# Performance work log

Measured on AMD Instinct MI355X. Metric: run time of the kernel, lower is better.

Reference implementation:

```python
import jax, jax.numpy as jnp
import numpy as np

N = 100000   # num_nodes
E = 1000000  # num_edges
H = 64       # h_dim
OUT = 16     # out_dim (num classes)
R = 90       # num_rels
B = 8        # num_bases


def setup_inputs() -> dict:
    key = jax.random.key(0)
    ks = jax.random.split(key, 16)
    feats = jax.random.normal(ks[0], (N, H), dtype=jnp.float32)
    src = jax.random.randint(ks[1], (E,), 0, N)
    dst = jax.random.randint(ks[2], (E,), 0, N)
    etype = jax.random.randint(ks[3], (E,), 0, R)
    norm = jax.random.uniform(ks[4], (E, 1), dtype=jnp.float32)
    s_in = 1.0 / np.sqrt(H)
    s_b = 1.0 / np.sqrt(B)
    # layer 0: H->H, layer 1 (hidden): H->H, layer 2: H->OUT
    coeff0 = jax.random.normal(ks[5], (R, B), dtype=jnp.float32) * s_b
    bases0 = jax.random.normal(ks[6], (B, H, H), dtype=jnp.float32) * s_in
    bias0 = jnp.zeros((H,), dtype=jnp.float32)
    coeff1 = jax.random.normal(ks[7], (R, B), dtype=jnp.float32) * s_b
    bases1 = jax.random.normal(ks[8], (B, H, H), dtype=jnp.float32) * s_in
    bias1 = jnp.zeros((H,), dtype=jnp.float32)
    coeff2 = jax.random.normal(ks[9], (R, B), dtype=jnp.float32) * s_b
    bases2 = jax.random.normal(ks[10], (B, H, OUT), dtype=jnp.float32) * s_in
    bias2 = jnp.zeros((OUT,), dtype=jnp.float32)
    return {
        "feats": feats,
        "coeff0": coeff0, "bases0": bases0, "bias0": bias0,
        "coeff1": coeff1, "bases1": bases1, "bias1": bias1,
        "coeff2": coeff2, "bases2": bases2, "bias2": bias2,
        "src": src, "dst": dst, "etype": etype, "norm": norm,
    }


def _rgcn_layer(x, coeff, bases, bias, src, dst, etype, norm, relu):
    # Basis decomposition: W_r = sum_b coeff[r,b] * bases[b]
    # Project all nodes through every basis once: [N, B, out]
    Hn = jnp.einsum('ni,bio->nbo', x, bases)
    c = coeff[etype]  # [E, B] per-edge basis coefficients
    # Per-edge message m_e = (sum_b c_eb * Hn[src_e, b]) * norm_e,
    # accumulated over the (small, fixed) basis dim to avoid an [E,B,out] buffer.
    m = c[:, 0:1] * Hn[src, 0]
    for b in range(1, bases.shape[0]):
        m = m + c[:, b:b + 1] * Hn[src, b]
    m = m * norm
    h = jax.ops.segment_sum(m, dst, num_segments=x.shape[0]) + bias
    return jax.nn.relu(h) if relu else h


def reference(feats, coeff0, bases0, bias0, coeff1, bases1, bias1,
              coeff2, bases2, bias2, src, dst, etype, norm):
    h = _rgcn_layer(feats, coeff0, bases0, bias0, src, dst, etype, norm, relu=True)
    h = _rgcn_layer(h, coeff1, bases1, bias1, src, dst, etype, norm, relu=True)
    h = _rgcn_layer(h, coeff2, bases2, bias2, src, dst, etype, norm, relu=False)
    return h
```

## Files before the change

kernel.cpp:

```cpp
#include <hip/hip_runtime.h>
#include <hip/hip_bf16.h>
#include <cstdint>

#define NNODES 100000
#define NEDGES 1000000
#define HDIM 64
#define ODIM 16
#define NB 8
#define KDIM (HDIM * NB)

typedef short short8 __attribute__((ext_vector_type(8)));
typedef float f32x4  __attribute__((ext_vector_type(4)));
union FragU { uint4 u; short8 s; };

__device__ __forceinline__ float asf(uint32_t u) { float f; __builtin_memcpy(&f, &u, 4); return f; }
__device__ __forceinline__ uint32_t asu(float f) { uint32_t u; __builtin_memcpy(&u, &f, 4); return u; }
__device__ __forceinline__ uint16_t f2bf(float f) {
    uint32_t x = asu(f);
    return (uint16_t)((x + 0x7FFFu + ((x >> 16) & 1u)) >> 16);
}
__device__ __forceinline__ uint32_t pack2(float lo, float hi) {
    return (uint32_t)f2bf(lo) | ((uint32_t)f2bf(hi) << 16);
}
__device__ __forceinline__ void fmaC(const float4& cA, const float4& cB, float xs,
                                     float* __restrict__ acc) {
    acc[0] = fmaf(cA.x, xs, acc[0]); acc[1] = fmaf(cA.y, xs, acc[1]);
    acc[2] = fmaf(cA.z, xs, acc[2]); acc[3] = fmaf(cA.w, xs, acc[3]);
    acc[4] = fmaf(cB.x, xs, acc[4]); acc[5] = fmaf(cB.y, xs, acc[5]);
    acc[6] = fmaf(cB.z, xs, acc[6]); acc[7] = fmaf(cB.w, xs, acc[7]);
}

__global__ void cast_kernel(const float* __restrict__ in, uint16_t* __restrict__ out, int n4) {
    const int stride = (int)(gridDim.x * blockDim.x);
    for (int idx = (int)(blockIdx.x * blockDim.x + threadIdx.x); idx < n4; idx += stride) {
        float4 v = reinterpret_cast<const float4*>(in)[idx];
        uint2 p;
        p.x = pack2(v.x, v.y);
        p.y = pack2(v.z, v.w);
        reinterpret_cast<uint2*>(out)[idx] = p;
    }
}

__global__ void zero_kernel(int* __restrict__ p, int n) {
    for (int i = (int)(blockIdx.x * blockDim.x + threadIdx.x); i < n;
         i += (int)(gridDim.x * blockDim.x)) p[i] = 0;
}

__global__ void hist_kernel(const int* __restrict__ dst, int* __restrict__ cnt, int nE) {
    for (int e = (int)(blockIdx.x * blockDim.x + threadIdx.x); e < nE;
         e += (int)(gridDim.x * blockDim.x)) atomicAdd(&cnt[dst[e]], 1);
}

#define SCAN_B 512
__launch_bounds__(SCAN_B)
__global__ void scan_partial_kernel(const int* __restrict__ cnt, int* __restrict__ bsum, int n) {
    __shared__ int sh[SCAN_B];
    int id = (int)(blockIdx.x * SCAN_B + threadIdx.x);
    sh[threadIdx.x] = (id < n) ? cnt[id] : 0;
    __syncthreads();
    for (int off = SCAN_B / 2; off > 0; off >>= 1) {
        if ((int)threadIdx.x < off) sh[threadIdx.x] += sh[threadIdx.x + off];
        __syncthreads();
    }
    if (threadIdx.x == 0) bsum[blockIdx.x] = sh[0];
}

__launch_bounds__(256)
__global__ void scan_base_kernel(const int* __restrict__ bsum, int* __restrict__ bbase,
                                 int* __restrict__ offs, int nblk, int nNodes) {
    __shared__ int sh[256];
    const int t = (int)threadIdx.x;
    int v = (t < nblk) ? bsum[t] : 0;
    sh[t] = v;
    __syncthreads();
    for (int off = 1; off < 256; off <<= 1) {
        int tmp = (t >= off) ? sh[t - off] : 0;
        __syncthreads();
        sh[t] += tmp;
        __syncthreads();
    }
    if (t < nblk) bbase[t] = sh[t] - v;
    if (t == 255) offs[nNodes] = sh[255];
}

__launch_bounds__(SCAN_B)
__global__ void scan_final_kernel(int* __restrict__ cnt, const int* __restrict__ bbase,
                                  int* __restrict__ offs, int n) {
    __shared__ int sh[SCAN_B];
    int id = (int)(blockIdx.x * SCAN_B + threadIdx.x);
    int v = (id < n) ? cnt[id] : 0;
    sh[threadIdx.x] = v;
    __syncthreads();
    for (int off = 1; off < SCAN_B; off <<= 1) {
        int tmp = ((int)threadIdx.x >= off) ? sh[threadIdx.x - off] : 0;
        __syncthreads();
        sh[threadIdx.x] += tmp;
        __syncthreads();
    }
    if (id < n) {
        int excl = sh[threadIdx.x] - v + bbase[blockIdx.x];
        offs[id] = excl;
        cnt[id]  = excl;
    }
}

__global__ void scatter_kernel(const int* __restrict__ src, const int* __restrict__ dst,
                               const int* __restrict__ et, const float* __restrict__ norm,
                               int* __restrict__ cursor, uint2* __restrict__ rec, int nE) {
    for (int e = (int)(blockIdx.x * blockDim.x + threadIdx.x); e < nE;
         e += (int)(gridDim.x * blockDim.x)) {
        int p = atomicAdd(&cursor[dst[e]], 1);
        rec[p] = make_uint2((uint32_t)src[e] | ((uint32_t)et[e] << 20), asu(norm[e]));
    }
}

__launch_bounds__(256)
__global__ void csr_agg_kernel(const uint16_t* __restrict__ x,
                               const float* __restrict__ coeff,
                               const int* __restrict__ offs,
                               const uint2* __restrict__ rec,
                               uint16_t* __restrict__ G, int nNodes) {
    const int hl   = (int)threadIdx.x & 31;
    const int hwid = (int)((blockIdx.x * blockDim.x + threadIdx.x) >> 5);
    const int nhw  = (int)((gridDim.x * blockDim.x) >> 5);
    for (int d = hwid; d < nNodes; d += nhw) {
        const int j0 = offs[d], j1 = offs[d + 1];
        float accL[NB] = {0.f, 0.f, 0.f, 0.f, 0.f, 0.f, 0.f, 0.f};
        float accH[NB] = {0.f, 0.f, 0.f, 0.f, 0.f, 0.f, 0.f, 0.f};
        int j = j0;
        for (; j + 4 <= j1; j += 4) {
            const uint2 r0 = rec[j];
            const uint2 r1 = rec[j + 1];
            const uint2 r2 = rec[j + 2];
            const uint2 r3 = rec[j + 3];
            const uint32_t w0 = *reinterpret_cast<const uint32_t*>(
                x + (size_t)(r0.x & 0xFFFFFu) * HDIM + 2 * hl);
            const uint32_t w1 = *reinterpret_cast<const uint32_t*>(
                x + (size_t)(r1.x & 0xFFFFFu) * HDIM + 2 * hl);
            const uint32_t w2 = *reinterpret_cast<const uint32_t*>(
                x + (size_t)(r2.x & 0xFFFFFu) * HDIM + 2 * hl);
            const uint32_t w3 = *reinterpret_cast<const uint32_t*>(
                x + (size_t)(r3.x & 0xFFFFFu) * HDIM + 2 * hl);

            {
                const float4 cA = *reinterpret_cast<const float4*>(coeff + (r0.x >> 20) * NB);
                const float4 cB = *reinterpret_cast<const float4*>(coeff + (r0.x >> 20) * NB + 4);
                const float nm = asf(r0.y);
                fmaC(cA, cB, asf(w0 << 16) * nm, accL);
                fmaC(cA, cB, asf(w0 & 0xFFFF0000u) * nm, accH);
            }
            {
                const float4 cA = *reinterpret_cast<const float4*>(coeff + (r1.x >> 20) * NB);
                const float4 cB = *reinterpret_cast<const float4*>(coeff + (r1.x >> 20) * NB + 4);
                const float nm = asf(r1.y);
                fmaC(cA, cB, asf(w1 << 16) * nm, accL);
                fmaC(cA, cB, asf(w1 & 0xFFFF0000u) * nm, accH);
            }
            {
                const float4 cA = *reinterpret_cast<const float4*>(coeff + (r2.x >> 20) * NB);
                const float4 cB = *reinterpret_cast<const float4*>(coeff + (r2.x >> 20) * NB + 4);
                const float nm = asf(r2.y);
                fmaC(cA, cB, asf(w2 << 16) * nm, accL);
                fmaC(cA, cB, asf(w2 & 0xFFFF0000u) * nm, accH);
            }
            {
                const float4 cA = *reinterpret_cast<const float4*>(coeff + (r3.x >> 20) * NB);
                const float4 cB = *reinterpret_cast<const float4*>(coeff + (r3.x >> 20) * NB + 4);
                const float nm = asf(r3.y);
                fmaC(cA, cB, asf(w3 << 16) * nm, accL);
                fmaC(cA, cB, asf(w3 & 0xFFFF0000u) * nm, accH);
            }
        }
        for (; j < j1; j++) {
            const uint2 r0 = rec[j];
            const uint32_t w0 = *reinterpret_cast<const uint32_t*>(
                x + (size_t)(r0.x & 0xFFFFFu) * HDIM + 2 * hl);
            const float4 cA = *reinterpret_cast<const float4*>(coeff + (r0.x >> 20) * NB);
            const float4 cB = *reinterpret_cast<const float4*>(coeff + (r0.x >> 20) * NB + 4);
            const float nm = asf(r0.y);
            fmaC(cA, cB, asf(w0 << 16) * nm, accL);
            fmaC(cA, cB, asf(w0 & 0xFFFF0000u) * nm, accH);
        }
        uint4 lo, hi;
        lo.x = pack2(accL[0], accL[1]); lo.y = pack2(accL[2], accL[3]);
        lo.z = pack2(accL[4], accL[5]); lo.w = pack2(accL[6], accL[7]);
        hi.x = pack2(accH[0], accH[1]); hi.y = pack2(accH[2], accH[3]);
        hi.z = pack2(accH[4], accH[5]); hi.w = pack2(accH[6], accH[7]);
        uint16_t* gp = G + (size_t)d * KDIM + hl * 16;
        *reinterpret_cast<uint4*>(gp)     = lo;
        *reinterpret_cast<uint4*>(gp + 8) = hi;
    }
}

__launch_bounds__(256)
__global__ void proj_hidden_kernel(const uint16_t* __restrict__ G,
                                   const float* __restrict__ bases,
                                   const float* __restrict__ bias,
                                   uint16_t* __restrict__ xout, int nNodes) {
    constexpr int OT = HDIM / 16;
    __shared__ __align__(16) uint16_t Wf[16 * OT * 64 * 8];

    const int t    = (int)threadIdx.x;
    const int lane = t & 63;
    const int w    = t >> 6;
    const int q    = lane >> 4;
    const int c    = lane & 15;

    for (int idx = t; idx < 16 * OT * 64 * 8; idx += 256) {
        int j    = idx & 7;
        int ln   = (idx >> 3) & 63;
        int rest = idx >> 9;
        int ot   = rest & (OT - 1);
        int kb   = rest >> 2;
        int k    = kb * 32 + (ln >> 4) * 8 + j;
        int o    = ot * 16 + (ln & 15);
        int i    = k >> 3, b = k & 7;
        Wf[idx] = f2bf(bases[(size_t)(b * HDIM + i) * HDIM + o]);
    }
    __syncthreads();

    float bv[OT];
#pragma unroll
    for (int ot = 0; ot < OT; ot++) bv[ot] = bias[ot * 16 + c];

    const int nTiles = (nNodes + 63) / 64;
    for (int tile = blockIdx.x; tile < nTiles; tile += gridDim.x) {
        const int n0w = tile * 64 + w * 16;
        int arow = n0w + c;
        if (arow > nNodes - 1) arow = nNodes - 1;
        const uint16_t* gp = G + (size_t)arow * KDIM + q * 8;

        f32x4 acc[OT];
#pragma unroll
        for (int ot = 0; ot < OT; ot++) acc[ot] = {0.f, 0.f, 0.f, 0.f};

#pragma unroll
        for (int kb = 0; kb < 16; kb++) {
            FragU a;
            a.u = *reinterpret_cast<const uint4*>(gp + kb * 32);
#pragma unroll
            for (int ot = 0; ot < OT; ot++) {
                FragU b;
                b.u = *reinterpret_cast<const uint4*>(Wf + ((kb * OT + ot) * 64 + lane) * 8);
                acc[ot] = __builtin_amdgcn_mfma_f32_16x16x32_bf16(a.s, b.s, acc[ot], 0, 0, 0);
            }
        }

#pragma unroll
        for (int r = 0; r < 4; r++) {
            const int node = n0w + q * 4 + r;
            if (node < nNodes) {
#pragma unroll
                for (int ot = 0; ot < OT; ot++) {
                    float v = fmaxf(acc[ot][r] + bv[ot], 0.f);
                    xout[(size_t)node * HDIM + ot * 16 + c] = f2bf(v);
                }
            }
        }
    }
}

__launch_bounds__(256)
__global__ void proj_out_kernel(const uint16_t* __restrict__ G,
                                const float* __restrict__ bases,
                                const float* __restrict__ bias,
                                float* __restrict__ out, int nNodes) {
    __shared__ __align__(16) uint16_t Wf[16 * 64 * 8];

    const int t    = (int)threadIdx.x;
    const int lane = t & 63;
    const int w    = t >> 6;
    const int q    = lane >> 4;
    const int c    = lane & 15;

    for (int idx = t; idx < 16 * 64 * 8; idx += 256) {
        int j  = idx & 7;
        int ln = (idx >> 3) & 63;
        int kb = idx >> 9;
        int k  = kb * 32 + (ln >> 4) * 8 + j;
        int o  = ln & 15;
        int i  = k >> 3, b = k & 7;
        Wf[idx] = f2bf(bases[(size_t)(b * HDIM + i) * ODIM + o]);
    }
    __syncthreads();

    const float bv = bias[c];

    const int nTiles = (nNodes + 63) / 64;
    for (int tile = blockIdx.x; tile < nTiles; tile += gridDim.x) {
        const int n0w = tile * 64 + w * 16;
        int arow = n0w + c;
        if (arow > nNodes - 1) arow = nNodes - 1;
        const uint16_t* gp = G + (size_t)arow * KDIM + q * 8;

        f32x4 acc = {0.f, 0.f, 0.f, 0.f};
#pragma unroll
        for (int kb = 0; kb < 16; kb++) {
            FragU a, b;
            a.u = *reinterpret_cast<const uint4*>(gp + kb * 32);
            b.u = *reinterpret_cast<const uint4*>(Wf + (kb * 64 + lane) * 8);
            acc = __builtin_amdgcn_mfma_f32_16x16x32_bf16(a.s, b.s, acc, 0, 0, 0);
        }

#pragma unroll
        for (int r = 0; r < 4; r++) {
            const int node = n0w + q * 4 + r;
            if (node < nNodes) out[(size_t)node * ODIM + c] = acc[r] + bv;
        }
    }
}

extern "C" void kernel_launch(void* const* d_in, const int* in_sizes, int n_in,
                              void* d_out, int out_size, void* d_ws, size_t ws_size,
                              hipStream_t stream) {
    const float* feats  = (const float*)d_in[0];
    const float* coeff0 = (const float*)d_in[1];
    const float* bases0 = (const float*)d_in[2];
    const float* bias0  = (const float*)d_in[3];
    const float* coeff1 = (const float*)d_in[4];
    const float* bases1 = (const float*)d_in[5];
    const float* bias1  = (const float*)d_in[6];
    const float* coeff2 = (const float*)d_in[7];
    const float* bases2 = (const float*)d_in[8];
    const float* bias2  = (const float*)d_in[9];
    const int*   src    = (const int*)d_in[10];
    const int*   dst    = (const int*)d_in[11];
    const int*   etype  = (const int*)d_in[12];
    const float* norm   = (const float*)d_in[13];
    float* out = (float*)d_out;

    char* base = (char*)d_ws;
    uint16_t* G = (uint16_t*)base;
    uint16_t* x = (uint16_t*)(base + (size_t)NNODES * KDIM * 2);
    const size_t OFF_OFFS  = 115200000;
    const size_t OFF_CURS  = OFF_OFFS + 400016;
    const size_t OFF_BSUM  = OFF_CURS + 400016;
    const size_t OFF_BBASE = OFF_BSUM + 1024;
    const size_t OFF_REC   = OFF_BBASE + 1024;
    int*   offs  = (int*)(base + OFF_OFFS);
    int*   curs  = (int*)(base + OFF_CURS);
    int*   bsum  = (int*)(base + OFF_BSUM);
    int*   bbase = (int*)(base + OFF_BBASE);
    uint2* rec   = (uint2*)(base + OFF_REC);

    const int nblk = (NNODES + SCAN_B - 1) / SCAN_B;

    hipLaunchKernelGGL(zero_kernel, dim3(256), dim3(256), 0, stream, curs, NNODES);
    hipLaunchKernelGGL(hist_kernel, dim3(2048), dim3(256), 0, stream, dst, curs, NEDGES);
    hipLaunchKernelGGL(scan_partial_kernel, dim3(nblk), dim3(SCAN_B), 0, stream, curs, bsum, NNODES);
    hipLaunchKernelGGL(scan_base_kernel, dim3(1), dim3(256), 0, stream, bsum, bbase, offs, nblk, NNODES);
    hipLaunchKernelGGL(scan_final_kernel, dim3(nblk), dim3(SCAN_B), 0, stream, curs, bbase, offs, NNODES);
    hipLaunchKernelGGL(scatter_kernel, dim3(2048), dim3(256), 0, stream,
                       src, dst, etype, norm, curs, rec, NEDGES);

    hipLaunchKernelGGL(cast_kernel, dim3(2048), dim3(256), 0, stream,
                       feats, x, NNODES * HDIM / 4);

    hipLaunchKernelGGL(csr_agg_kernel, dim3(2048), dim3(256), 0, stream,
                       x, coeff0, offs, rec, G, NNODES);
    hipLaunchKernelGGL(proj_hidden_kernel, dim3(512), dim3(256), 0, stream,
                       G, bases0, bias0, x, NNODES);
    hipLaunchKernelGGL(csr_agg_kernel, dim3(2048), dim3(256), 0, stream,
                       x, coeff1, offs, rec, G, NNODES);
    hipLaunchKernelGGL(proj_hidden_kernel, dim3(512), dim3(256), 0, stream,
                       G, bases1, bias1, x, NNODES);
    hipLaunchKernelGGL(csr_agg_kernel, dim3(2048), dim3(256), 0, stream,
                       x, coeff2, offs, rec, G, NNODES);
    hipLaunchKernelGGL(proj_out_kernel, dim3(512), dim3(256), 0, stream,
                       G, bases2, bias2, out, NNODES);
}
```

Measured before the change: 534.2 us.

## Fuse CSR gather aggregation with MFMA basis projection via shared-memory tile

Merges the per-node gather/aggregate kernel and the basis projection GEMM into one kernel per layer. Each 1024-thread block aggregates 64 destination nodes into a swizzled LDS tile and then runs MFMA on it. This removes the write and reread of the large [N, 512] bf16 intermediate in global memory. It adds block-wide barriers and uses large blocks with about 80KB of LDS, which may limit occupancy and let slow nodes with many edges stall their whole block. Ping-pong buffers xA and xB replace the in-place x update.

```diff
diff --git a/kernel.cpp b/kernel.cpp
--- a/kernel.cpp
+++ b/kernel.cpp
@@ -8,6 +8,7 @@
 #define ODIM 16
 #define NB 8
 #define KDIM (HDIM * NB)
+#define TILE 64
 
 typedef short short8 __attribute__((ext_vector_type(8)));
 typedef float f32x4  __attribute__((ext_vector_type(4)));
@@ -114,166 +115,171 @@
     }
 }
 
-__launch_bounds__(256)
-__global__ void csr_agg_kernel(const uint16_t* __restrict__ x,
-                               const float* __restrict__ coeff,
-                               const int* __restrict__ offs,
-                               const uint2* __restrict__ rec,
-                               uint16_t* __restrict__ G, int nNodes) {
-    const int hl   = (int)threadIdx.x & 31;
-    const int hwid = (int)((blockIdx.x * blockDim.x + threadIdx.x) >> 5);
-    const int nhw  = (int)((gridDim.x * blockDim.x) >> 5);
-    for (int d = hwid; d < nNodes; d += nhw) {
-        const int j0 = offs[d], j1 = offs[d + 1];
-        float accL[NB] = {0.f, 0.f, 0.f, 0.f, 0.f, 0.f, 0.f, 0.f};
-        float accH[NB] = {0.f, 0.f, 0.f, 0.f, 0.f, 0.f, 0.f, 0.f};
-        int j = j0;
-        for (; j + 4 <= j1; j += 4) {
-            const uint2 r0 = rec[j];
-            const uint2 r1 = rec[j + 1];
-            const uint2 r2 = rec[j + 2];
-            const uint2 r3 = rec[j + 3];
-            const uint32_t w0 = *reinterpret_cast<const uint32_t*>(
-                x + (size_t)(r0.x & 0xFFFFFu) * HDIM + 2 * hl);
-            const uint32_t w1 = *reinterpret_cast<const uint32_t*>(
-                x + (size_t)(r1.x & 0xFFFFFu) * HDIM + 2 * hl);
-            const uint32_t w2 = *reinterpret_cast<const uint32_t*>(
-                x + (size_t)(r2.x & 0xFFFFFu) * HDIM + 2 * hl);
-            const uint32_t w3 = *reinterpret_cast<const uint32_t*>(
-                x + (size_t)(r3.x & 0xFFFFFu) * HDIM + 2 * hl);
-
-            {
-                const float4 cA = *reinterpret_cast<const float4*>(coeff + (r0.x >> 20) * NB);
-                const float4 cB = *reinterpret_cast<const float4*>(coeff + (r0.x >> 20) * NB + 4);
-                const float nm = asf(r0.y);
-                fmaC(cA, cB, asf(w0 << 16) * nm, accL);
-                fmaC(cA, cB, asf(w0 & 0xFFFF0000u) * nm, accH);
-            }
-            {
-                const float4 cA = *reinterpret_cast<const float4*>(coeff + (r1.x >> 20) * NB);
-                const float4 cB = *reinterpret_cast<const float4*>(coeff + (r1.x >> 20) * NB + 4);
-                const float nm = asf(r1.y);
-                fmaC(cA, cB, asf(w1 << 16) * nm, accL);
-                fmaC(cA, cB, asf(w1 & 0xFFFF0000u) * nm, accH);
-            }
-            {
-                const float4 cA = *reinterpret_cast<const float4*>(coeff + (r2.x >> 20) * NB);
-                const float4 cB = *reinterpret_cast<const float4*>(coeff + (r2.x >> 20) * NB + 4);
-                const float nm = asf(r2.y);
-                fmaC(cA, cB, asf(w2 << 16) * nm, accL);
-                fmaC(cA, cB, asf(w2 & 0xFFFF0000u) * nm, accH);
-            }
-            {
-                const float4 cA = *reinterpret_cast<const float4*>(coeff + (r3.x >> 20) * NB);
-                const float4 cB = *reinterpret_cast<const float4*>(coeff + (r3.x >> 20) * NB + 4);
-                const float nm = asf(r3.y);
-                fmaC(cA, cB, asf(w3 << 16) * nm, accL);
-                fmaC(cA, cB, asf(w3 & 0xFFFF0000u) * nm, accH);
-            }
-        }
-        for (; j < j1; j++) {
-            const uint2 r0 = rec[j];
-            const uint32_t w0 = *reinterpret_cast<const uint32_t*>(
-                x + (size_t)(r0.x & 0xFFFFFu) * HDIM + 2 * hl);
+__device__ __forceinline__ void gather_node(const uint16_t* __restrict__ x,
+                                            const float* __restrict__ coeff,
+                                            const uint2* __restrict__ rec,
+                                            int j0, int j1, int hl,
+                                            float* __restrict__ accL,
+                                            float* __restrict__ accH) {
+    int j = j0;
+    for (; j + 4 <= j1; j += 4) {
+        const uint2 r0 = rec[j];
+        const uint2 r1 = rec[j + 1];
+        const uint2 r2 = rec[j + 2];
+        const uint2 r3 = rec[j + 3];
+        const uint32_t w0 = *reinterpret_cast<const uint32_t*>(
+            x + (size_t)(r0.x & 0xFFFFFu) * HDIM + 2 * hl);
+        const uint32_t w1 = *reinterpret_cast<const uint32_t*>(
+            x + (size_t)(r1.x & 0xFFFFFu) * HDIM + 2 * hl);
+        const uint32_t w2 = *reinterpret_cast<const uint32_t*>(
+            x + (size_t)(r2.x & 0xFFFFFu) * HDIM + 2 * hl);
+        const uint32_t w3 = *reinterpret_cast<const uint32_t*>(
+            x + (size_t)(r3.x & 0xFFFFFu) * HDIM + 2 * hl);
+        {
             const float4 cA = *reinterpret_cast<const float4*>(coeff + (r0.x >> 20) * NB);
             const float4 cB = *reinterpret_cast<const float4*>(coeff + (r0.x >> 20) * NB + 4);
             const float nm = asf(r0.y);
             fmaC(cA, cB, asf(w0 << 16) * nm, accL);
             fmaC(cA, cB, asf(w0 & 0xFFFF0000u) * nm, accH);
         }
-        uint4 lo, hi;
-        lo.x = pack2(accL[0], accL[1]); lo.y = pack2(accL[2], accL[3]);
-        lo.z = pack2(accL[4], accL[5]); lo.w = pack2(accL[6], accL[7]);
-        hi.x = pack2(accH[0], accH[1]); hi.y = pack2(accH[2], accH[3]);
-        hi.z = pack2(accH[4], accH[5]); hi.w = pack2(accH[6], accH[7]);
-        uint16_t* gp = G + (size_t)d * KDIM + hl * 16;
-        *reinterpret_cast<uint4*>(gp)     = lo;
-        *reinterpret_cast<uint4*>(gp + 8) = hi;
-    }
-}
-
-__launch_bounds__(256)
-__global__ void proj_hidden_kernel(const uint16_t* __restrict__ G,
-                                   const float* __restrict__ bases,
-                                   const float* __restrict__ bias,
-                                   uint16_t* __restrict__ xout, int nNodes) {
+        {
+            const float4 cA = *reinterpret_cast<const float4*>(coeff + (r1.x >> 20) * NB);
+            const float4 cB = *reinterpret_cast<const float4*>(coeff + (r1.x >> 20) * NB + 4);
+            const float nm = asf(r1.y);
+            fmaC(cA, cB, asf(w1 << 16) * nm, accL);
+            fmaC(cA, cB, asf(w1 & 0xFFFF0000u) * nm, accH);
+        }
+        {
+            const float4 cA = *reinterpret_cast<const float4*>(coeff + (r2.x >> 20) * NB);
+            const float4 cB = *reinterpret_cast<const float4*>(coeff + (r2.x >> 20) * NB + 4);
+            const float nm = asf(r2.y);
+            fmaC(cA, cB, asf(w2 << 16) * nm, accL);
+            fmaC(cA, cB, asf(w2 & 0xFFFF0000u) * nm, accH);
+        }
+        {
+            const float4 cA = *reinterpret_cast<const float4*>(coeff + (r3.x >> 20) * NB);
+            const float4 cB = *reinterpret_cast<const float4*>(coeff + (r3.x >> 20) * NB + 4);
+            const float nm = asf(r3.y);
+            fmaC(cA, cB, asf(w3 << 16) * nm, accL);
+            fmaC(cA, cB, asf(w3 & 0xFFFF0000u) * nm, accH);
+        }
+    }
+    for (; j < j1; j++) {
+        const uint2 r0 = rec[j];
+        const uint32_t w0 = *reinterpret_cast<const uint32_t*>(
+            x + (size_t)(r0.x & 0xFFFFFu) * HDIM + 2 * hl);
+        const float4 cA = *reinterpret_cast<const float4*>(coeff + (r0.x >> 20) * NB);
+        const float4 cB = *reinterpret_cast<const float4*>(coeff + (r0.x >> 20) * NB + 4);
+        const float nm = asf(r0.y);
+        fmaC(cA, cB, asf(w0 << 16) * nm, accL);
+        fmaC(cA, cB, asf(w0 & 0xFFFF0000u) * nm, accH);
+    }
+}
+
+__launch_bounds__(1024)
+__global__ void fused_hidden_kernel(const uint16_t* __restrict__ x,
+                                    const float* __restrict__ coeff,
+                                    const float* __restrict__ bases,
+                                    const float* __restrict__ bias,
+                                    const int* __restrict__ offs,
+                                    const uint2* __restrict__ rec,
+                                    uint16_t* __restrict__ xout, int nNodes) {
     constexpr int OT = HDIM / 16;
     __shared__ __align__(16) uint16_t Wf[16 * OT * 64 * 8];
+    __shared__ __align__(16) uint16_t Gs[TILE * KDIM];
 
     const int t    = (int)threadIdx.x;
     const int lane = t & 63;
     const int w    = t >> 6;
+    const int hw   = t >> 5;
+    const int hl   = t & 31;
     const int q    = lane >> 4;
     const int c    = lane & 15;
-
-    for (int idx = t; idx < 16 * OT * 64 * 8; idx += 256) {
+    const int rt   = w & 3;
+    const int ot   = w >> 2;
+
+    for (int idx = t; idx < 16 * OT * 64 * 8; idx += 1024) {
         int j    = idx & 7;
         int ln   = (idx >> 3) & 63;
         int rest = idx >> 9;
-        int ot   = rest & (OT - 1);
+        int o_t  = rest & (OT - 1);
         int kb   = rest >> 2;
         int k    = kb * 32 + (ln >> 4) * 8 + j;
-        int o    = ot * 16 + (ln & 15);
+        int o    = o_t * 16 + (ln & 15);
         int i    = k >> 3, b = k & 7;
         Wf[idx] = f2bf(bases[(size_t)(b * HDIM + i) * HDIM + o]);
     }
-    __syncthreads();
-
-    float bv[OT];
-#pragma unroll
-    for (int ot = 0; ot < OT; ot++) bv[ot] = bias[ot * 16 + c];
-
-    const int nTiles = (nNodes + 63) / 64;
-    for (int tile = blockIdx.x; tile < nTiles; tile += gridDim.x) {
-        const int n0w = tile * 64 + w * 16;
-        int arow = n0w + c;
-        if (arow > nNodes - 1) arow = nNodes - 1;
-        const uint16_t* gp = G + (size_t)arow * KDIM + q * 8;
-
-        f32x4 acc[OT];
-#pragma unroll
-        for (int ot = 0; ot < OT; ot++) acc[ot] = {0.f, 0.f, 0.f, 0.f};
-
+
+    const float bv = bias[ot * 16 + c];
+    const int rsw  = rt * 16 + c;
+    const uint16_t* arow = Gs + rsw * KDIM;
+    const int sw   = rsw & 7;
+
+    const int nTiles = (nNodes + TILE - 1) / TILE;
+    for (int tile = (int)blockIdx.x; tile < nTiles; tile += (int)gridDim.x) {
+#pragma unroll
+        for (int s = 0; s < 2; s++) {
+            const int r = hw * 2 + s;
+            const int d = tile * TILE + r;
+            if (d < nNodes) {
+                float accL[NB] = {0.f, 0.f, 0.f, 0.f, 0.f, 0.f, 0.f, 0.f};
+                float accH[NB] = {0.f, 0.f, 0.f, 0.f, 0.f, 0.f, 0.f, 0.f};
+                gather_node(x, coeff, rec, offs[d], offs[d + 1], hl, accL, accH);
+                uint4 lo, hi;
+                lo.x = pack2(accL[0], accL[1]); lo.y = pack2(accL[2], accL[3]);
+                lo.z = pack2(accL[4], accL[5]); lo.w = pack2(accL[6], accL[7]);
+                hi.x = pack2(accH[0], accH[1]); hi.y = pack2(accH[2], accH[3]);
+                hi.z = pack2(accH[4], accH[5]); hi.w = pack2(accH[6], accH[7]);
+                uint16_t* gp = Gs + r * KDIM;
+                *reinterpret_cast<uint4*>(gp + ((hl ^ (r & 7)) * 8))        = lo;
+                *reinterpret_cast<uint4*>(gp + (((32 + hl) ^ (r & 7)) * 8)) = hi;
+            }
+        }
+        __syncthreads();
+
+        f32x4 acc = {0.f, 0.f, 0.f, 0.f};
 #pragma unroll
         for (int kb = 0; kb < 16; kb++) {
-            FragU a;
-            a.u = *reinterpret_cast<const uint4*>(gp + kb * 32);
-#pragma unroll
-            for (int ot = 0; ot < OT; ot++) {
-                FragU b;
-                b.u = *reinterpret_cast<const uint4*>(Wf + ((kb * OT + ot) * 64 + lane) * 8);
-                acc[ot] = __builtin_amdgcn_mfma_f32_16x16x32_bf16(a.s, b.s, acc[ot], 0, 0, 0);
-            }
-        }
-
-#pragma unroll
-        for (int r = 0; r < 4; r++) {
-            const int node = n0w + q * 4 + r;
+            const int g0 = (q & 1) * 32 + 2 * kb + (q >> 1);
+            FragU a, b;
+            a.u = *reinterpret_cast<const uint4*>(arow + ((g0 ^ sw) * 8));
+            b.u = *reinterpret_cast<const uint4*>(Wf + ((kb * OT + ot) * 64 + lane) * 8);
+            acc = __builtin_amdgcn_mfma_f32_16x16x32_bf16(a.s, b.s, acc, 0, 0, 0);
+        }
+
+        const int nbase = tile * TILE + rt * 16 + q * 4;
+#pragma unroll
+        for (int ri = 0; ri < 4; ri++) {
+            const int node = nbase + ri;
             if (node < nNodes) {
-#pragma unroll
-                for (int ot = 0; ot < OT; ot++) {
-                    float v = fmaxf(acc[ot][r] + bv[ot], 0.f);
-                    xout[(size_t)node * HDIM + ot * 16 + c] = f2bf(v);
-                }
-            }
-        }
-    }
-}
-
-__launch_bounds__(256)
-__global__ void proj_out_kernel(const uint16_t* __restrict__ G,
-                                const float* __restrict__ bases,
-                                const float* __restrict__ bias,
-                                float* __restrict__ out, int nNodes) {
+                float v = fmaxf(acc[ri] + bv, 0.f);
+                xout[(size_t)node * HDIM + ot * 16 + c] = f2bf(v);
+            }
+        }
+        __syncthreads();
+    }
+}
+
+__launch_bounds__(1024)
+__global__ void fused_out_kernel(const uint16_t* __restrict__ x,
+                                 const float* __restrict__ coeff,
+                                 const float* __restrict__ bases,
+                                 const float* __restrict__ bias,
+                                 const int* __restrict__ offs,
+                                 const uint2* __restrict__ rec,
+                                 float* __restrict__ out, int nNodes) {
     __shared__ __align__(16) uint16_t Wf[16 * 64 * 8];
+    __shared__ __align__(16) uint16_t Gs[TILE * KDIM];
 
     const int t    = (int)threadIdx.x;
     const int lane = t & 63;
     const int w    = t >> 6;
+    const int hw   = t >> 5;
+    const int hl   = t & 31;
     const int q    = lane >> 4;
     const int c    = lane & 15;
 
-    for (int idx = t; idx < 16 * 64 * 8; idx += 256) {
+    for (int idx = t; idx < 16 * 64 * 8; idx += 1024) {
         int j  = idx & 7;
         int ln = (idx >> 3) & 63;
         int kb = idx >> 9;
@@ -282,31 +288,53 @@
         int i  = k >> 3, b = k & 7;
         Wf[idx] = f2bf(bases[(size_t)(b * HDIM + i) * ODIM + o]);
     }
-    __syncthreads();
 
     const float bv = bias[c];
-
-    const int nTiles = (nNodes + 63) / 64;
-    for (int tile = blockIdx.x; tile < nTiles; tile += gridDim.x) {
-        const int n0w = tile * 64 + w * 16;
-        int arow = n0w + c;
-        if (arow > nNodes - 1) arow = nNodes - 1;
-        const uint16_t* gp = G + (size_t)arow * KDIM + q * 8;
-
-        f32x4 acc = {0.f, 0.f, 0.f, 0.f};
-#pragma unroll
-        for (int kb = 0; kb < 16; kb++) {
-            FragU a, b;
-            a.u = *reinterpret_cast<const uint4*>(gp + kb * 32);
-            b.u = *reinterpret_cast<const uint4*>(Wf + (kb * 64 + lane) * 8);
-            acc = __builtin_amdgcn_mfma_f32_16x16x32_bf16(a.s, b.s, acc, 0, 0, 0);
-        }
-
-#pragma unroll
-        for (int r = 0; r < 4; r++) {
-            const int node = n0w + q * 4 + r;
-            if (node < nNodes) out[(size_t)node * ODIM + c] = acc[r] + bv;
-        }
+    const int rt   = w & 3;
+    const int rsw  = rt * 16 + c;
+    const uint16_t* arow = Gs + rsw * KDIM;
+    const int sw   = rsw & 7;
+
+    const int nTiles = (nNodes + TILE - 1) / TILE;
+    for (int tile = (int)blockIdx.x; tile < nTiles; tile += (int)gridDim.x) {
+#pragma unroll
+        for (int s = 0; s < 2; s++) {
+            const int r = hw * 2 + s;
+            const int d = tile * TILE + r;
+            if (d < nNodes) {
+                float accL[NB] = {0.f, 0.f, 0.f, 0.f, 0.f, 0.f, 0.f, 0.f};
+                float accH[NB] = {0.f, 0.f, 0.f, 0.f, 0.f, 0.f, 0.f, 0.f};
+                gather_node(x, coeff, rec, offs[d], offs[d + 1], hl, accL, accH);
+                uint4 lo, hi;
+                lo.x = pack2(accL[0], accL[1]); lo.y = pack2(accL[2], accL[3]);
+                lo.z = pack2(accL[4], accL[5]); lo.w = pack2(accL[6], accL[7]);
+                hi.x = pack2(accH[0], accH[1]); hi.y = pack2(accH[2], accH[3]);
+                hi.z = pack2(accH[4], accH[5]); hi.w = pack2(accH[6], accH[7]);
+                uint16_t* gp = Gs + r * KDIM;
+                *reinterpret_cast<uint4*>(gp + ((hl ^ (r & 7)) * 8))        = lo;
+                *reinterpret_cast<uint4*>(gp + (((32 + hl) ^ (r & 7)) * 8)) = hi;
+            }
+        }
+        __syncthreads();
+
+        if (w < 4) {
+            f32x4 acc = {0.f, 0.f, 0.f, 0.f};
+#pragma unroll
+            for (int kb = 0; kb < 16; kb++) {
+                const int g0 = (q & 1) * 32 + 2 * kb + (q >> 1);
+                FragU a, b;
+                a.u = *reinterpret_cast<const uint4*>(arow + ((g0 ^ sw) * 8));
+                b.u = *reinterpret_cast<const uint4*>(Wf + ((kb * 64 + lane) * 8));
+                acc = __builtin_amdgcn_mfma_f32_16x16x32_bf16(a.s, b.s, acc, 0, 0, 0);
+            }
+            const int nbase = tile * TILE + rt * 16 + q * 4;
+#pragma unroll
+            for (int ri = 0; ri < 4; ri++) {
+                const int node = nbase + ri;
+                if (node < nNodes) out[(size_t)node * ODIM + c] = acc[ri] + bv;
+            }
+        }
+        __syncthreads();
     }
 }
 
@@ -330,8 +358,8 @@
     float* out = (float*)d_out;
 
     char* base = (char*)d_ws;
-    uint16_t* G = (uint16_t*)base;
-    uint16_t* x = (uint16_t*)(base + (size_t)NNODES * KDIM * 2);
+    uint16_t* xA = (uint16_t*)base;
+    uint16_t* xB = (uint16_t*)(base + (size_t)NNODES * HDIM * 2);
     const size_t OFF_OFFS  = 115200000;
     const size_t OFF_CURS  = OFF_OFFS + 400016;
     const size_t OFF_BSUM  = OFF_CURS + 400016;
@@ -354,18 +382,12 @@
                        src, dst, etype, norm, curs, rec, NEDGES);
 
     hipLaunchKernelGGL(cast_kernel, dim3(2048), dim3(256), 0, stream,
-                       feats, x, NNODES * HDIM / 4);
-
-    hipLaunchKernelGGL(csr_agg_kernel, dim3(2048), dim3(256), 0, stream,
-                       x, coeff0, offs, rec, G, NNODES);
-    hipLaunchKernelGGL(proj_hidden_kernel, dim3(512), dim3(256), 0, stream,
-                       G, bases0, bias0, x, NNODES);
-    hipLaunchKernelGGL(csr_agg_kernel, dim3(2048), dim3(256), 0, stream,
-                       x, coeff1, offs, rec, G, NNODES);
-    hipLaunchKernelGGL(proj_hidden_kernel, dim3(512), dim3(256), 0, stream,
-                       G, bases1, bias1, x, NNODES);
-    hipLaunchKernelGGL(csr_agg_kernel, dim3(2048), dim3(256), 0, stream,
-                       x, coeff2, offs, rec, G, NNODES);
-    hipLaunchKernelGGL(proj_out_kernel, dim3(512), dim3(256), 0, stream,
-                       G, bases2, bias2, out, NNODES);
-}
+                       feats, xA, NNODES * HDIM / 4);
+
+    hipLaunchKernelGGL(fused_hidden_kernel, dim3(512), dim3(1024), 0, stream,
+                       xA, coeff0, bases0, bias0, offs, rec, xB, NNODES);
+    hipLaunchKernelGGL(fused_hidden_kernel, dim3(512), dim3(1024), 0, stream,
+                       xB, coeff1, bases1, bias1, offs, rec, xA, NNODES);
+    hipLaunchKernelGGL(fused_out_kernel, dim3(512), dim3(1024), 0, stream,
+                       xA, coeff2, bases2, bias2, offs, rec, out, NNODES);
+}
```

New measurement: 537.0 us. No clear change (+0.5%).

## Hold projection weights in registers and split output tiles across waves

Applied to the files above, without the earlier changes.

The projection kernels stop staging bf16 basis weights in LDS and instead load each wave's B fragments straight into registers. In proj_hidden each wave now owns one 16-column output tile and loops over four 16-row node groups, rather than each wave computing all four output tiles for its own rows. Launch bounds gain a minimum-occupancy hint and the grids double to 1024 blocks. The goal is to drop LDS reads and the setup barrier, at the cost of higher register pressure and each wave reading the G rows four times (likely served by cache).

```diff
diff --git a/kernel.cpp b/kernel.cpp
--- a/kernel.cpp
+++ b/kernel.cpp
@@ -7,6 +7,7 @@
 #define HDIM 64
 #define ODIM 16
 #define NB 8
+#define NREL 90
 #define KDIM (HDIM * NB)
 
 typedef short short8 __attribute__((ext_vector_type(8)));
@@ -192,119 +193,99 @@
     }
 }
 
-__launch_bounds__(256)
+__launch_bounds__(256, 3)
 __global__ void proj_hidden_kernel(const uint16_t* __restrict__ G,
                                    const float* __restrict__ bases,
                                    const float* __restrict__ bias,
                                    uint16_t* __restrict__ xout, int nNodes) {
-    constexpr int OT = HDIM / 16;
-    __shared__ __align__(16) uint16_t Wf[16 * OT * 64 * 8];
-
+    const int t    = (int)threadIdx.x;
+    const int lane = t & 63;
+    const int ot   = t >> 6;
+    const int q    = lane >> 4;
+    const int c    = lane & 15;
+
+    FragU bf[16];
+#pragma unroll
+    for (int kb = 0; kb < 16; kb++) {
+#pragma unroll
+        for (int j = 0; j < 8; j++) {
+            const int k = kb * 32 + q * 8 + j;
+            const int i = k >> 3, b = k & 7;
+            bf[kb].s[j] = (short)f2bf(bases[(size_t)(b * HDIM + i) * HDIM + ot * 16 + c]);
+        }
+    }
+    const float bv = bias[ot * 16 + c];
+
+    const int nTiles = (nNodes + 63) / 64;
+    for (int tile = (int)blockIdx.x; tile < nTiles; tile += (int)gridDim.x) {
+#pragma unroll
+        for (int g = 0; g < 4; g++) {
+            int arow = tile * 64 + g * 16 + c;
+            if (arow > nNodes - 1) arow = nNodes - 1;
+            const uint16_t* gp = G + (size_t)arow * KDIM + q * 8;
+
+            f32x4 acc = {0.f, 0.f, 0.f, 0.f};
+#pragma unroll
+            for (int kb = 0; kb < 16; kb++) {
+                FragU a;
+                a.u = *reinterpret_cast<const uint4*>(gp + kb * 32);
+                acc = __builtin_amdgcn_mfma_f32_16x16x32_bf16(a.s, bf[kb].s, acc, 0, 0, 0);
+            }
+
+            const int nbase = tile * 64 + g * 16 + q * 4;
+#pragma unroll
+            for (int r = 0; r < 4; r++) {
+                const int node = nbase + r;
+                if (node < nNodes) {
+                    float v = fmaxf(acc[r] + bv, 0.f);
+                    xout[(size_t)node * HDIM + ot * 16 + c] = f2bf(v);
+                }
+            }
+        }
+    }
+}
+
+__launch_bounds__(256, 3)
+__global__ void proj_out_kernel(const uint16_t* __restrict__ G,
+                                const float* __restrict__ bases,
+                                const float* __restrict__ bias,
+                                float* __restrict__ out, int nNodes) {
     const int t    = (int)threadIdx.x;
     const int lane = t & 63;
     const int w    = t >> 6;
     const int q    = lane >> 4;
     const int c    = lane & 15;
 
-    for (int idx = t; idx < 16 * OT * 64 * 8; idx += 256) {
-        int j    = idx & 7;
-        int ln   = (idx >> 3) & 63;
-        int rest = idx >> 9;
-        int ot   = rest & (OT - 1);
-        int kb   = rest >> 2;
-        int k    = kb * 32 + (ln >> 4) * 8 + j;
-        int o    = ot * 16 + (ln & 15);
-        int i    = k >> 3, b = k & 7;
-        Wf[idx] = f2bf(bases[(size_t)(b * HDIM + i) * HDIM + o]);
-    }
-    __syncthreads();
-
-    float bv[OT];
-#pragma unroll
-    for (int ot = 0; ot < OT; ot++) bv[ot] = bias[ot * 16 + c];
+    FragU bf[16];
+#pragma unroll
+    for (int kb = 0; kb < 16; kb++) {
+#pragma unroll
+        for (int j = 0; j < 8; j++) {
+            const int k = kb * 32 + q * 8 + j;
+            const int i = k >> 3, b = k & 7;
+            bf[kb].s[j] = (short)f2bf(bases[(size_t)(b * HDIM + i) * ODIM + c]);
+        }
+    }
+    const float bv = bias[c];
 
     const int nTiles = (nNodes + 63) / 64;
-    for (int tile = blockIdx.x; tile < nTiles; tile += gridDim.x) {
-        const int n0w = tile * 64 + w * 16;
-        int arow = n0w + c;
+    for (int tile = (int)blockIdx.x; tile < nTiles; tile += (int)gridDim.x) {
+        int arow = tile * 64 + w * 16 + c;
         if (arow > nNodes - 1) arow = nNodes - 1;
         const uint16_t* gp = G + (size_t)arow * KDIM + q * 8;
 
-        f32x4 acc[OT];
-#pragma unroll
-        for (int ot = 0; ot < OT; ot++) acc[ot] = {0.f, 0.f, 0.f, 0.f};
-
+        f32x4 acc = {0.f, 0.f, 0.f, 0.f};
 #pragma unroll
         for (int kb = 0; kb < 16; kb++) {
             FragU a;
             a.u = *reinterpret_cast<const uint4*>(gp + kb * 32);
-#pragma unroll
-            for (int ot = 0; ot < OT; ot++) {
-                FragU b;
-                b.u = *reinterpret_cast<const uint4*>(Wf + ((kb * OT + ot) * 64 + lane) * 8);
-                acc[ot] = __builtin_amdgcn_mfma_f32_16x16x32_bf16(a.s, b.s, acc[ot], 0, 0, 0);
-            }
-        }
-
+            acc = __builtin_amdgcn_mfma_f32_16x16x32_bf16(a.s, bf[kb].s, acc, 0, 0, 0);
+        }
+
+        const int nbase = tile * 64 + w * 16 + q * 4;
 #pragma unroll
         for (int r = 0; r < 4; r++) {
-            const int node = n0w + q * 4 + r;
-            if (node < nNodes) {
-#pragma unroll
-                for (int ot = 0; ot < OT; ot++) {
-                    float v = fmaxf(acc[ot][r] + bv[ot], 0.f);
-                    xout[(size_t)node * HDIM + ot * 16 + c] = f2bf(v);
-                }
-            }
-        }
-    }
-}
-
-__launch_bounds__(256)
-__global__ void proj_out_kernel(const uint16_t* __restrict__ G,
-                                const float* __restrict__ bases,
-                                const float* __restrict__ bias,
-                                float* __restrict__ out, int nNodes) {
-    __shared__ __align__(16) uint16_t Wf[16 * 64 * 8];
-
-    const int t    = (int)threadIdx.x;
-    const int lane = t & 63;
-    const int w    = t >> 6;
-    const int q    = lane >> 4;
-    const int c    = lane & 15;
-
-    for (int idx = t; idx < 16 * 64 * 8; idx += 256) {
-        int j  = idx & 7;
-        int ln = (idx >> 3) & 63;
-        int kb = idx >> 9;
-        int k  = kb * 32 + (ln >> 4) * 8 + j;
-        int o  = ln & 15;
-        int i  = k >> 3, b = k & 7;
-        Wf[idx] = f2bf(bases[(size_t)(b * HDIM + i) * ODIM + o]);
-    }
-    __syncthreads();
-
-    const float bv = bias[c];
-
-    const int nTiles = (nNodes + 63) / 64;
-    for (int tile = blockIdx.x; tile < nTiles; tile += gridDim.x) {
-        const int n0w = tile * 64 + w * 16;
-        int arow = n0w + c;
-        if (arow > nNodes - 1) arow = nNodes - 1;
-        const uint16_t* gp = G + (size_t)arow * KDIM + q * 8;
-
-        f32x4 acc = {0.f, 0.f, 0.f, 0.f};
-#pragma unroll
-        for (int kb = 0; kb < 16; kb++) {
-            FragU a, b;
-            a.u = *reinterpret_cast<const uint4*>(gp + kb * 32);
-            b.u = *reinterpret_cast<const uint4*>(Wf + (kb * 64 + lane) * 8);
-            acc = __builtin_amdgcn_mfma_f32_16x16x32_bf16(a.s, b.s, acc, 0, 0, 0);
-        }
-
-#pragma unroll
-        for (int r = 0; r < 4; r++) {
-            const int node = n0w + q * 4 + r;
+            const int node = nbase + r;
             if (node < nNodes) out[(size_t)node * ODIM + c] = acc[r] + bv;
         }
     }
@@ -358,14 +339,14 @@
 
     hipLaunchKernelGGL(csr_agg_kernel, dim3(2048), dim3(256), 0, stream,
                        x, coeff0, offs, rec, G, NNODES);
-    hipLaunchKernelGGL(proj_hidden_kernel, dim3(512), dim3(256), 0, stream,
+    hipLaunchKernelGGL(proj_hidden_kernel, dim3(1024), dim3(256), 0, stream,
                        G, bases0, bias0, x, NNODES);
     hipLaunchKernelGGL(csr_agg_kernel, dim3(2048), dim3(256), 0, stream,
                        x, coeff1, offs, rec, G, NNODES);
-    hipLaunchKernelGGL(proj_hidden_kernel, dim3(512), dim3(256), 0, stream,
+    hipLaunchKernelGGL(proj_hidden_kernel, dim3(1024), dim3(256), 0, stream,
                        G, bases1, bias1, x, NNODES);
     hipLaunchKernelGGL(csr_agg_kernel, dim3(2048), dim3(256), 0, stream,
                        x, coeff2, offs, rec, G, NNODES);
-    hipLaunchKernelGGL(proj_out_kernel, dim3(512), dim3(256), 0, stream,
+    hipLaunchKernelGGL(proj_out_kernel, dim3(1024), dim3(256), 0, stream,
                        G, bases2, bias2, out, NNODES);
 }
```

Result: slower. 553.5 us (+3.6%).
